# Kernel optimization log

Measured on AMD Instinct MI355X. Metric: run time of the kernel, lower is better.

The kernel has to match this reference:

```python
import jax, jax.numpy as jnp
import numpy as np

B, S, E, H = 4, 1024, 1024, 16
D = E // H  # 64


def setup_inputs() -> dict:
    key = jax.random.key(0)
    ks = jax.random.split(key, 11)
    scale = 1.0 / np.sqrt(E)
    inp = {
        "q": jax.random.normal(ks[0], (B, S, E), jnp.float32),
        "k": jax.random.normal(ks[1], (B, S, E), jnp.float32),
        "v": jax.random.normal(ks[2], (B, S, E), jnp.float32),
        "mask": jax.random.randint(ks[3], (B, 1, 1, S), 0, 2, jnp.int32),
        # torch.nn.Linear params: W is [out, in], y = x @ W.T + b
        "Wq": jax.random.uniform(ks[4], (E, E), jnp.float32, -scale, scale),
        "bq": jax.random.uniform(ks[5], (E,), jnp.float32, -scale, scale),
        "Wk": jax.random.uniform(ks[6], (E, E), jnp.float32, -scale, scale),
        "bk": jax.random.uniform(ks[7], (E,), jnp.float32, -scale, scale),
        "Wo": jax.random.uniform(ks[8], (E, E), jnp.float32, -scale, scale),
        "bo": jax.random.uniform(ks[9], (E,), jnp.float32, -scale, scale),
    }
    return inp


def reference(q, k, v, mask, Wq, bq, Wk, bk, Wo, bo):
    # Projections. NOTE: original code applies key_linear to v (value_linear unused).
    qh = (q @ Wq.T + bq).reshape(B, S, H, D).transpose(0, 2, 1, 3)  # [B,H,S,D]
    kh = (k @ Wk.T + bk).reshape(B, S, H, D).transpose(0, 2, 1, 3)
    vh = (v @ Wk.T + bk).reshape(B, S, H, D).transpose(0, 2, 1, 3)

    scores = jnp.einsum("bhqd,bhkd->bhqk", qh, kh) / jnp.sqrt(jnp.float32(D))
    pad = mask == 0  # [B,1,1,S] broadcast
    scores = jnp.where(pad, jnp.float32(-1e9), scores)
    attn = jax.nn.softmax(scores, axis=-1)
    attn = jnp.where(pad, jnp.float32(0.0), attn)

    ctx = jnp.einsum("bhqk,bhkd->bhqd", attn, vh)  # [B,H,S,D]
    ctx = ctx.transpose(0, 2, 1, 3).reshape(B, S, E)
    return ctx @ Wo.T + bo
```

## Files before the change

kernel.cpp:

```cpp
#include <hip/hip_runtime.h>

typedef unsigned short u16;
typedef unsigned int   u32;
typedef __attribute__((ext_vector_type(8))) short bf16x8;
typedef __attribute__((ext_vector_type(4))) float f32x4;
typedef __attribute__((ext_vector_type(4))) u32   u32x4;

#define MFMA(a,b,c) __builtin_amdgcn_mfma_f32_16x16x32_bf16(a,b,c,0,0,0)


__device__ __forceinline__ u32 cvtpk(float lo, float hi){
  u32 r; asm("v_cvt_pk_bf16_f32 %0, %1, %2" : "=v"(r) : "v"(lo), "v"(hi)); return r;
}
__device__ __forceinline__ u16 f2bf(float f){ return (u16)cvtpk(f,f); }
__device__ __forceinline__ bf16x8 cvt8(f32x4 lo, f32x4 hi){
  u32x4 u;
  u.x = cvtpk(lo[0],lo[1]); u.y = cvtpk(lo[2],lo[3]);
  u.z = cvtpk(hi[0],hi[1]); u.w = cvtpk(hi[2],hi[3]);
  return *(bf16x8*)&u;
}

__device__ __forceinline__ int swz(int row, int col){
  return (((row<<6) + col)<<1) ^ ((row&7)<<4);
}

__device__ __forceinline__ void gl16(const void* g, void* l){
  __builtin_amdgcn_global_load_lds(
      (const __attribute__((address_space(1))) u32*)g,
      (__attribute__((address_space(3))) u32*)l, 16, 0, 0);
}

template<int ROWS>
__device__ __forceinline__ void stage_bf16(const u16* g, size_t ldg, char* lds, int wv, int lane){
  #pragma unroll
  for (int i=0;i<ROWS/32;++i){
    const int r0 = wv*(ROWS/4) + (i<<3);
    const int row = r0 + (lane>>3);
    const int c = ((lane&7) ^ (row&7)) << 3;
    gl16(g + (size_t)row*ldg + c, lds + (r0<<7));
  }
}

__device__ __forceinline__ bf16x8 frag_bf16(const char* lds, int row, int kcol){
  return *(const bf16x8*)(lds + swz(row,kcol));
}

__global__ __launch_bounds__(256) void prep_k(
    const float* __restrict__ wq, const float* __restrict__ wk, const float* __restrict__ wo,
    const float* __restrict__ q,  const float* __restrict__ k,  const float* __restrict__ v,
    u16* __restrict__ out,
    const int* __restrict__ mask, int* __restrict__ scat, int* __restrict__ cnts)
{
  const int tid = threadIdx.x;
  if (blockIdx.x < 7680){
    const size_t i8 = (((size_t)blockIdx.x<<8) + tid) << 3;
    const float* src;
    if      (i8 <  1048576u) src = wq + i8;
    else if (i8 <  2097152u) src = wk + (i8 - 1048576u);
    else if (i8 <  3145728u) src = wo + (i8 - 2097152u);
    else if (i8 <  7340032u) src = q  + (i8 - 3145728u);
    else if (i8 < 11534336u) src = k  + (i8 - 7340032u);
    else                     src = v  + (i8 - 11534336u);
    f32x4 lo = *(const f32x4*)src, hi = *(const f32x4*)(src+4);
    *(bf16x8*)(out + i8) = cvt8(lo, hi);
  } else {
    const int b = blockIdx.x - 7680, lane = tid&63, wv = tid>>6;
    __shared__ int wsum[4];
    const int4 m = *(const int4*)(mask + (b<<10) + (tid<<2));
    const int c0 = (m.x!=0)+(m.y!=0)+(m.z!=0)+(m.w!=0);
    int pre = c0;
    #pragma unroll
    for (int i=1;i<64;i<<=1){
      int t = __shfl_up(pre, i);
      if (lane >= i) pre += t;
    }
    if (lane==63) wsum[wv] = pre;
    __syncthreads();
    int base = pre - c0;
    #pragma unroll
    for (int w=0;w<4;++w) if (w<wv) base += wsum[w];
    int p = base;
    int* sb = scat + (b<<10) + (tid<<2);
    sb[0] = m.x ? p++ : -1;
    sb[1] = m.y ? p++ : -1;
    sb[2] = m.z ? p++ : -1;
    sb[3] = m.w ? p++ : -1;
    if (tid==255) cnts[b] = p;
  }
}

template<int V>
__device__ __forceinline__ void proj_body(
    int m0, int n0, const u16* __restrict__ Aa, const u16* __restrict__ Bb,
    const float* __restrict__ bias, u16* __restrict__ outb, const int* __restrict__ sc,
    char* As, char* Bs)
{
  constexpr int NT = 4;
  const int tid = threadIdx.x, lane = tid&63, wv = tid>>6;
  const int wm = wv>>1, wn = wv&1, l15 = lane&15, g4 = lane>>4;

  f32x4 acc[4][NT] = {};

  #pragma unroll 1
  for (int kt=0; kt<1024; kt+=64){
    __syncthreads();
    stage_bf16<128>(Aa + (size_t)m0*1024 + kt, 1024, As, wv, lane);
    stage_bf16<128>(Bb + (size_t)n0*1024 + kt, 1024, Bs, wv, lane);
    __syncthreads();

    #pragma unroll
    for (int kb=0;kb<64;kb+=32){
      const int kcol = kb + (g4<<3);
      bf16x8 af[4], bf_[NT];
      #pragma unroll
      for (int t=0;t<4;++t)
        af[t] = frag_bf16(As, (wm<<6) + (t<<4) + l15, kcol);
      #pragma unroll
      for (int t=0;t<NT;++t)
        bf_[t] = frag_bf16(Bs, (wn<<6) + (t<<4) + l15, kcol);
      #pragma unroll
      for (int mt=0;mt<4;++mt)
        #pragma unroll
        for (int nt=0;nt<NT;++nt)
          acc[mt][nt] = MFMA(af[mt], bf_[nt], acc[mt][nt]);
    }
  }

  f32x4 bmv[4];
  if (V==1){
    #pragma unroll
    for (int mt=0;mt<4;++mt)
      bmv[mt] = *(const f32x4*)(bias + m0 + (wm<<6) + (mt<<4) + (g4<<2));
  }
  int drow[4][4];
  if (V==0){
    #pragma unroll
    for (int mt=0;mt<4;++mt)
      #pragma unroll
      for (int j=0;j<4;++j){
        const int m = m0 + (wm<<6) + (mt<<4) + (g4<<2) + j;
        int d = m;
        if (sc){ const int c = sc[m]; d = (c<0) ? -1 : ((m & ~1023) | c); }
        drow[mt][j] = d;
      }
  }
  int dcol[NT];
  if (V==1){
    #pragma unroll
    for (int nt=0;nt<NT;++nt){
      const int col = n0 + (wn<<6) + (nt<<4) + l15;
      const int c = sc[col];
      dcol[nt] = (c<0) ? -1 : ((col & ~1023) | c);
    }
  }

  #pragma unroll
  for (int nt=0;nt<NT;++nt){
    const int col = n0 + (wn<<6) + (nt<<4) + l15;
    const float bvn = (V==1) ? 0.f : bias[col];
    #pragma unroll
    for (int mt=0;mt<4;++mt){
      const int mb = m0 + (wm<<6) + (mt<<4) + (g4<<2);
      f32x4 a = acc[mt][nt];
      #pragma unroll
      for (int j=0;j<4;++j){
        const float val = a[j] + ((V==1) ? bmv[mt][j] : bvn);
        if (V==1){ if (dcol[nt]>=0)     outb[(size_t)(mb+j)*4096 + dcol[nt]] = f2bf(val); }
        else      { if (drow[mt][j]>=0) outb[(size_t)drow[mt][j]*1024 + col] = f2bf(val); }
      }
    }
  }
}

__global__ __launch_bounds__(256,4) void proj_k(
    const u16* __restrict__ qb, const u16* __restrict__ kb, const u16* __restrict__ vb,
    const u16* __restrict__ wqb, const u16* __restrict__ wkb,
    const float* __restrict__ bq, const float* __restrict__ bk,
    u16* __restrict__ qp, u16* __restrict__ kp, u16* __restrict__ vt,
    const int* __restrict__ scat)
{
  __shared__ __align__(16) char As[16384];
  __shared__ __align__(16) char Bs[16384];
  const int bid = blockIdx.x;
  if (bid < 512){
    const int z = bid>>8, local = bid&255;
    proj_body<0>((local&31)<<7, ((local>>5)&7)<<7,
                 z?kb:qb, z?wkb:wqb, z?bk:bq, z?kp:qp, z?scat:nullptr, As, Bs);
  } else {
    const int local = bid-512;
    proj_body<1>((local&7)<<7, (local>>3)<<7, wkb, vb, bk, vt, scat, As, Bs);
  }
}

__global__ __launch_bounds__(256,4) void oproj_k(
    const u16* __restrict__ ctx, const u16* __restrict__ wob,
    const float* __restrict__ bo, float* __restrict__ of)
{
  constexpr int BN = 64, NT = 2;
  __shared__ __align__(16) char As[16384];
  __shared__ __align__(16) char Bs[BN*128];
  const int m0 = blockIdx.x<<7, n0 = blockIdx.y*BN;
  const int tid = threadIdx.x, lane = tid&63, wv = tid>>6;
  const int wm = wv>>1, wn = wv&1, l15 = lane&15, g4 = lane>>4;

  f32x4 acc[4][NT] = {};

  #pragma unroll 1
  for (int kt=0; kt<1024; kt+=64){
    __syncthreads();
    stage_bf16<128>(ctx + (size_t)m0*1024 + kt, 1024, As, wv, lane);
    stage_bf16<BN> (wob + (size_t)n0*1024 + kt, 1024, Bs, wv, lane);
    __syncthreads();

    #pragma unroll
    for (int kb=0;kb<64;kb+=32){
      const int kcol = kb + (g4<<3);
      bf16x8 af[4], bf_[NT];
      #pragma unroll
      for (int t=0;t<4;++t)
        af[t] = frag_bf16(As, (wm<<6) + (t<<4) + l15, kcol);
      #pragma unroll
      for (int t=0;t<NT;++t)
        bf_[t] = frag_bf16(Bs, wn*(BN>>1) + (t<<4) + l15, kcol);
      #pragma unroll
      for (int mt=0;mt<4;++mt)
        #pragma unroll
        for (int nt=0;nt<NT;++nt)
          acc[mt][nt] = MFMA(af[mt], bf_[nt], acc[mt][nt]);
    }
  }

  #pragma unroll
  for (int nt=0;nt<NT;++nt){
    const int col = n0 + wn*(BN>>1) + (nt<<4) + l15;
    const float bvn = bo[col];
    #pragma unroll
    for (int mt=0;mt<4;++mt){
      const int mb = m0 + (wm<<6) + (mt<<4) + (g4<<2);
      f32x4 a = acc[mt][nt];
      #pragma unroll
      for (int j=0;j<4;++j)
        of[(size_t)(mb+j)*1024 + col] = a[j] + bvn;
    }
  }
}

__global__ __launch_bounds__(256) void attn_k(
    const u16* __restrict__ qp, const u16* __restrict__ kp, const u16* __restrict__ vt,
    const int* __restrict__ cnts, u16* __restrict__ ctx)
{
  const int bid = blockIdx.x;
  const int wg  = (bid&7)*64 + (bid>>3);
  const int qt = wg&7, h = (wg>>3)&15, b = wg>>7;

  __shared__ __align__(16) u16 Qs[128*64];
  __shared__ __align__(16) u16 Ks[2][64*64];
  __shared__ __align__(16) u16 Vs[2][64*64];
  __shared__ __align__(16) u16 Ps[4*32*64];

  const int tid = threadIdx.x, lane = tid&63, wv = tid>>6;
  const int hc = h<<6, l15 = lane&15;
  const float C2 = 0.18033688011112042f;

  const int cnt = cnts[b];
  const int ntiles = (cnt + 63) >> 6;

  {
    const u16* Qg = qp + ((size_t)((b<<10) + (qt<<7)))*1024 + hc;
    #pragma unroll
    for (int i=0;i<4;++i){
      const int r0 = (wv<<5) + (i<<3);
      const int row = r0 + (lane>>3);
      const int c = ((lane&7) ^ (row&7)) << 3;
      gl16(Qg + (size_t)row*1024 + c, (char*)Qs + (r0<<7));
    }
  }

  const u16* Kg = kp + ((size_t)(b<<10))*1024 + hc;
  const u16* Vg = vt + ((size_t)hc)*4096 + (b<<10);

  auto stageKV = [&](int kt2, int bi){
    #pragma unroll
    for (int i=0;i<2;++i){
      const int r0 = (wv<<4) + (i<<3);
      const int row = r0 + (lane>>3);
      const int c = ((lane&7) ^ (row&7)) << 3;
      gl16(Kg + (size_t)((kt2<<6) + row)*1024 + c, (char*)Ks[bi] + (r0<<7));
      gl16(Vg + (size_t)row*4096 + (kt2<<6) + c,  (char*)Vs[bi] + (r0<<7));
    }
  };
  stageKV(0, 0);
  __syncthreads();

  f32x4 o[2][4] = {};
  float lr[2][4] = {};
  u16* Pw = Ps + (wv<<11);
  int cur = 0;

  #pragma unroll 1
  for (int kt=0; kt<ntiles; ++kt){
    if (kt+1 < ntiles) stageKV(kt+1, cur^1);
    const char* Kc = (const char*)Ks[cur];
    const char* Vc = (const char*)Vs[cur];

    f32x4 sc[2][4] = {};
    #pragma unroll
    for (int kb=0;kb<64;kb+=32){
      const int kcol = kb + ((lane>>4)<<3);
      bf16x8 kf[4];
      #pragma unroll
      for (int nt=0;nt<4;++nt) kf[nt] = frag_bf16(Kc, (nt<<4)+l15, kcol);
      bf16x8 aq0 = frag_bf16((const char*)Qs, (wv<<5)+l15, kcol);
      bf16x8 aq1 = frag_bf16((const char*)Qs, (wv<<5)+16+l15, kcol);
      __builtin_amdgcn_s_setprio(1);
      #pragma unroll
      for (int nt=0;nt<4;++nt) sc[0][nt] = MFMA(aq0, kf[nt], sc[0][nt]);
      #pragma unroll
      for (int nt=0;nt<4;++nt) sc[1][nt] = MFMA(aq1, kf[nt], sc[1][nt]);
      __builtin_amdgcn_s_setprio(0);
    }

    float bv4[4];
    #pragma unroll
    for (int nt=0;nt<4;++nt)
      bv4[nt] = ((kt<<6)+(nt<<4)+l15 < cnt) ? 0.f : -1e30f;
    #pragma unroll
    for (int sub=0;sub<2;++sub)
      #pragma unroll
      for (int nt=0;nt<4;++nt){
        f32x4 s = sc[sub][nt];
        #pragma unroll
        for (int j=0;j<4;++j){
          const float p = __builtin_amdgcn_exp2f(fmaf(s[j], C2, bv4[nt]));
          lr[sub][j] += p;
          *(u16*)((char*)Pw + swz((sub<<4)+((lane>>4)<<2)+j, (nt<<4)+l15)) = f2bf(p);
        }
      }
    asm volatile("s_waitcnt lgkmcnt(0)" ::: "memory");
    __builtin_amdgcn_sched_barrier(0);

    #pragma unroll
    for (int kb=0;kb<64;kb+=32){
      const int kcol = kb + ((lane>>4)<<3);
      bf16x8 vf[4];
      #pragma unroll
      for (int nt=0;nt<4;++nt) vf[nt] = frag_bf16(Vc, (nt<<4)+l15, kcol);
      bf16x8 pa0 = frag_bf16((const char*)Pw, l15, kcol);
      bf16x8 pa1 = frag_bf16((const char*)Pw, 16+l15, kcol);
      __builtin_amdgcn_s_setprio(1);
      #pragma unroll
      for (int nt=0;nt<4;++nt) o[0][nt] = MFMA(pa0, vf[nt], o[0][nt]);
      #pragma unroll
      for (int nt=0;nt<4;++nt) o[1][nt] = MFMA(pa1, vf[nt], o[1][nt]);
      __builtin_amdgcn_s_setprio(0);
    }
    __syncthreads();
    cur ^= 1;
  }

  #pragma unroll
  for (int sub=0;sub<2;++sub)
    #pragma unroll
    for (int j=0;j<4;++j){
      float s = lr[sub][j];
      s += __shfl_xor(s,1); s += __shfl_xor(s,2);
      s += __shfl_xor(s,4); s += __shfl_xor(s,8);
      const float inv = 1.f / fmaxf(s, 1e-30f);
      const int row = (qt<<7) + (wv<<5) + (sub<<4) + ((lane>>4)<<2) + j;
      u16* crow = ctx + ((size_t)((b<<10)+row))*1024 + hc;
      #pragma unroll
      for (int nt=0;nt<4;++nt)
        crow[(nt<<4)+l15] = f2bf(o[sub][nt][j]*inv);
    }
}

extern "C" void kernel_launch(void* const* d_in, const int* in_sizes, int n_in,
                              void* d_out, int out_size, void* d_ws, size_t ws_size,
                              hipStream_t stream) {
  const float* q    = (const float*)d_in[0];
  const float* k    = (const float*)d_in[1];
  const float* v    = (const float*)d_in[2];
  const int*   mask = (const int*)  d_in[3];
  const float* Wq   = (const float*)d_in[4];
  const float* bq   = (const float*)d_in[5];
  const float* Wk   = (const float*)d_in[6];
  const float* bk   = (const float*)d_in[7];
  const float* Wo   = (const float*)d_in[8];
  const float* bo   = (const float*)d_in[9];
  float* out = (float*)d_out;

  char* ws = (char*)d_ws;
  u16* wqb  = (u16*)(ws);
  u16* wkb  = (u16*)(ws +  2097152);
  u16* wob  = (u16*)(ws +  4194304);
  u16* qb   = (u16*)(ws +  6291456);
  u16* kb   = (u16*)(ws + 14680064);
  u16* vb   = (u16*)(ws + 23068672);
  u16* qp   = (u16*)(ws + 31457280);
  u16* kp   = (u16*)(ws + 39845888);
  u16* vtb  = (u16*)(ws + 48234496);
  u16* ctxb = (u16*)(ws + 56623104);
  int* scat = (int*)(ws + 65011712);
  int* cnts = (int*)(ws + 65028096);

  dim3 blk(256);
  prep_k<<<7684, blk, 0, stream>>>(Wq, Wk, Wo, q, k, v, wqb, mask, scat, cnts);
  proj_k<<<768, blk, 0, stream>>>(qb, kb, vb, wqb, wkb, bq, bk, qp, kp, vtb, scat);
  attn_k<<<512, blk, 0, stream>>>(qp, kp, vtb, cnts, ctxb);
  oproj_k<<<dim3(32,16), blk, 0, stream>>>(ctxb, wob, bo, out);
}
```

Baseline: 90.34 us.

## Gather unmasked rows before K/V projection and skip fully-masked tiles

Changes the mask compaction from a scatter map to a gather index list. The K and V projection GEMMs now load only unmasked rows through per-row gather addresses and write compacted outputs contiguously. Blocks whose tile lies beyond the per-batch valid count exit early, which removes about half of the K/V projection work under a random mask. Gathered global loads may coalesce less well, and the zero-filled index tail means padded rows of a partial tile compute on row 0.

```diff
diff --git a/kernel.cpp b/kernel.cpp
--- a/kernel.cpp
+++ b/kernel.cpp
@@ -49,7 +49,7 @@
     const float* __restrict__ wq, const float* __restrict__ wk, const float* __restrict__ wo,
     const float* __restrict__ q,  const float* __restrict__ k,  const float* __restrict__ v,
     u16* __restrict__ out,
-    const int* __restrict__ mask, int* __restrict__ scat, int* __restrict__ cnts)
+    const int* __restrict__ mask, int* __restrict__ gidx, int* __restrict__ cnts)
 {
   const int tid = threadIdx.x;
   if (blockIdx.x < 7680){
@@ -66,6 +66,8 @@
   } else {
     const int b = blockIdx.x - 7680, lane = tid&63, wv = tid>>6;
     __shared__ int wsum[4];
+    int4 z4; z4.x=0; z4.y=0; z4.z=0; z4.w=0;
+    *(int4*)(gidx + (b<<10) + (tid<<2)) = z4;
     const int4 m = *(const int4*)(mask + (b<<10) + (tid<<2));
     const int c0 = (m.x!=0)+(m.y!=0)+(m.z!=0)+(m.w!=0);
     int pre = c0;
@@ -80,48 +82,67 @@
     #pragma unroll
     for (int w=0;w<4;++w) if (w<wv) base += wsum[w];
     int p = base;
-    int* sb = scat + (b<<10) + (tid<<2);
-    sb[0] = m.x ? p++ : -1;
-    sb[1] = m.y ? p++ : -1;
-    sb[2] = m.z ? p++ : -1;
-    sb[3] = m.w ? p++ : -1;
+    const int s0 = tid<<2;
+    if (m.x) gidx[(b<<10) + p++] = s0;
+    if (m.y) gidx[(b<<10) + p++] = s0+1;
+    if (m.z) gidx[(b<<10) + p++] = s0+2;
+    if (m.w) gidx[(b<<10) + p++] = s0+3;
     if (tid==255) cnts[b] = p;
   }
 }
 
-template<int V>
+template<int V, bool GA, bool GB>
 __device__ __forceinline__ void proj_body(
-    int m0, int n0, const u16* __restrict__ Aa, const u16* __restrict__ Bb,
-    const float* __restrict__ bias, u16* __restrict__ outb, const int* __restrict__ sc,
+    const u16* __restrict__ Aa, const u16* __restrict__ Bb,
+    const int* __restrict__ gA, const int* __restrict__ gB,
+    const float* __restrict__ bias, u16* __restrict__ outb,
     char* As, char* Bs)
 {
-  constexpr int NT = 4;
   const int tid = threadIdx.x, lane = tid&63, wv = tid>>6;
   const int wm = wv>>1, wn = wv&1, l15 = lane&15, g4 = lane>>4;
 
-  f32x4 acc[4][NT] = {};
+  int growA[4], growB[4];
+  if (GA){
+    #pragma unroll
+    for (int i=0;i<4;++i) growA[i] = gA[(wv<<5)+(i<<3)+(lane>>3)] & 1023;
+  }
+  if (GB){
+    #pragma unroll
+    for (int i=0;i<4;++i) growB[i] = gB[(wv<<5)+(i<<3)+(lane>>3)] & 1023;
+  }
+
+  f32x4 acc[4][4] = {};
 
   #pragma unroll 1
   for (int kt=0; kt<1024; kt+=64){
     __syncthreads();
-    stage_bf16<128>(Aa + (size_t)m0*1024 + kt, 1024, As, wv, lane);
-    stage_bf16<128>(Bb + (size_t)n0*1024 + kt, 1024, Bs, wv, lane);
+    #pragma unroll
+    for (int i=0;i<4;++i){
+      const int r0 = (wv<<5)+(i<<3), row = r0+(lane>>3);
+      const int c = ((lane&7)^(row&7))<<3;
+      const u16* srcA = GA ? Aa + (size_t)growA[i]*1024 + kt + c
+                           : Aa + (size_t)row*1024 + kt + c;
+      gl16(srcA, As + (r0<<7));
+      const u16* srcB = GB ? Bb + (size_t)growB[i]*1024 + kt + c
+                           : Bb + (size_t)row*1024 + kt + c;
+      gl16(srcB, Bs + (r0<<7));
+    }
     __syncthreads();
 
     #pragma unroll
     for (int kb=0;kb<64;kb+=32){
       const int kcol = kb + (g4<<3);
-      bf16x8 af[4], bf_[NT];
+      bf16x8 af[4], bf_[4];
       #pragma unroll
       for (int t=0;t<4;++t)
         af[t] = frag_bf16(As, (wm<<6) + (t<<4) + l15, kcol);
       #pragma unroll
-      for (int t=0;t<NT;++t)
+      for (int t=0;t<4;++t)
         bf_[t] = frag_bf16(Bs, (wn<<6) + (t<<4) + l15, kcol);
       #pragma unroll
       for (int mt=0;mt<4;++mt)
         #pragma unroll
-        for (int nt=0;nt<NT;++nt)
+        for (int nt=0;nt<4;++nt)
           acc[mt][nt] = MFMA(af[mt], bf_[nt], acc[mt][nt]);
     }
   }
@@ -130,43 +151,21 @@
   if (V==1){
     #pragma unroll
     for (int mt=0;mt<4;++mt)
-      bmv[mt] = *(const f32x4*)(bias + m0 + (wm<<6) + (mt<<4) + (g4<<2));
-  }
-  int drow[4][4];
-  if (V==0){
-    #pragma unroll
-    for (int mt=0;mt<4;++mt)
+      bmv[mt] = *(const f32x4*)(bias + (wm<<6) + (mt<<4) + (g4<<2));
+  }
+  #pragma unroll
+  for (int nt=0;nt<4;++nt){
+    const int col = (wn<<6) + (nt<<4) + l15;
+    const float bvn = (V==1) ? 0.f : bias[col];
+    #pragma unroll
+    for (int mt=0;mt<4;++mt){
+      f32x4 a = acc[mt][nt];
       #pragma unroll
       for (int j=0;j<4;++j){
-        const int m = m0 + (wm<<6) + (mt<<4) + (g4<<2) + j;
-        int d = m;
-        if (sc){ const int c = sc[m]; d = (c<0) ? -1 : ((m & ~1023) | c); }
-        drow[mt][j] = d;
-      }
-  }
-  int dcol[NT];
-  if (V==1){
-    #pragma unroll
-    for (int nt=0;nt<NT;++nt){
-      const int col = n0 + (wn<<6) + (nt<<4) + l15;
-      const int c = sc[col];
-      dcol[nt] = (c<0) ? -1 : ((col & ~1023) | c);
-    }
-  }
-
-  #pragma unroll
-  for (int nt=0;nt<NT;++nt){
-    const int col = n0 + (wn<<6) + (nt<<4) + l15;
-    const float bvn = (V==1) ? 0.f : bias[col];
-    #pragma unroll
-    for (int mt=0;mt<4;++mt){
-      const int mb = m0 + (wm<<6) + (mt<<4) + (g4<<2);
-      f32x4 a = acc[mt][nt];
-      #pragma unroll
-      for (int j=0;j<4;++j){
+        const int ml = (wm<<6) + (mt<<4) + (g4<<2) + j;
         const float val = a[j] + ((V==1) ? bmv[mt][j] : bvn);
-        if (V==1){ if (dcol[nt]>=0)     outb[(size_t)(mb+j)*4096 + dcol[nt]] = f2bf(val); }
-        else      { if (drow[mt][j]>=0) outb[(size_t)drow[mt][j]*1024 + col] = f2bf(val); }
+        if (V==1) outb[(size_t)ml*4096 + col] = f2bf(val);
+        else      outb[(size_t)ml*1024 + col] = f2bf(val);
       }
     }
   }
@@ -177,18 +176,31 @@
     const u16* __restrict__ wqb, const u16* __restrict__ wkb,
     const float* __restrict__ bq, const float* __restrict__ bk,
     u16* __restrict__ qp, u16* __restrict__ kp, u16* __restrict__ vt,
-    const int* __restrict__ scat)
+    const int* __restrict__ gidx, const int* __restrict__ cnts)
 {
   __shared__ __align__(16) char As[16384];
   __shared__ __align__(16) char Bs[16384];
   const int bid = blockIdx.x;
-  if (bid < 512){
-    const int z = bid>>8, local = bid&255;
-    proj_body<0>((local&31)<<7, ((local>>5)&7)<<7,
-                 z?kb:qb, z?wkb:wqb, z?bk:bq, z?kp:qp, z?scat:nullptr, As, Bs);
+  if (bid < 256){
+    const int m0 = (bid&31)<<7, n0 = ((bid>>5)&7)<<7;
+    proj_body<0,false,false>(qb + (size_t)m0*1024, wqb + (size_t)n0*1024, nullptr, nullptr,
+                             bq + n0, qp + (size_t)m0*1024 + n0, As, Bs);
+  } else if (bid < 512){
+    const int local = bid-256;
+    const int m0 = (local&31)<<7, n0 = ((local>>5)&7)<<7;
+    const int b = m0>>10, mloc = m0&1023;
+    if (mloc >= cnts[b]) return;
+    proj_body<0,true,false>(kb + ((size_t)(b<<10))*1024, wkb + (size_t)n0*1024,
+                            gidx + (b<<10) + mloc, nullptr,
+                            bk + n0, kp + ((size_t)((b<<10)+mloc))*1024 + n0, As, Bs);
   } else {
     const int local = bid-512;
-    proj_body<1>((local&7)<<7, (local>>3)<<7, wkb, vb, bk, vt, scat, As, Bs);
+    const int m0 = (local&7)<<7, n0 = (local>>3)<<7;
+    const int b = n0>>10, nloc = n0&1023;
+    if (nloc >= cnts[b]) return;
+    proj_body<1,false,true>(wkb + (size_t)m0*1024, vb + ((size_t)(b<<10))*1024,
+                            nullptr, gidx + (b<<10) + nloc,
+                            bk + m0, vt + (size_t)m0*4096 + (b<<10) + nloc, As, Bs);
   }
 }
 
@@ -400,12 +412,12 @@
   u16* kp   = (u16*)(ws + 39845888);
   u16* vtb  = (u16*)(ws + 48234496);
   u16* ctxb = (u16*)(ws + 56623104);
-  int* scat = (int*)(ws + 65011712);
+  int* gidx = (int*)(ws + 65011712);
   int* cnts = (int*)(ws + 65028096);
 
   dim3 blk(256);
-  prep_k<<<7684, blk, 0, stream>>>(Wq, Wk, Wo, q, k, v, wqb, mask, scat, cnts);
-  proj_k<<<768, blk, 0, stream>>>(qb, kb, vb, wqb, wkb, bq, bk, qp, kp, vtb, scat);
+  prep_k<<<7684, blk, 0, stream>>>(Wq, Wk, Wo, q, k, v, wqb, mask, gidx, cnts);
+  proj_k<<<768, blk, 0, stream>>>(qb, kb, vb, wqb, wkb, bq, bk, qp, kp, vtb, gidx, cnts);
   attn_k<<<512, blk, 0, stream>>>(qp, kp, vtb, cnts, ctxb);
   oproj_k<<<dim3(32,16), blk, 0, stream>>>(ctxb, wob, bo, out);
 }
```

After: 84.54 us. 1.07x faster.
